# Kernel tuning notes

Measured on AMD Instinct MI355X. Metric: run time of the kernel, lower is better.

## Reference

```python
import jax, jax.numpy as jnp
import numpy as np

S, N_SUB, E_SUB = 64, 1024, 16384       # subgraphs, nodes/subgraph, edges/subgraph
N, E = 65536, 1048576                   # global nodes / edges
F_IN, NHID, NCLS, HEADS = 128, 128, 64, 2
RATIO = 0.5
K = int(np.ceil(RATIO * N_SUB))         # SAGPooling keeps K=512 nodes


def setup_inputs() -> dict:
    key = jax.random.key(0)
    ks = jax.random.split(key, 12)
    def lin(k, i, o):
        return jax.random.normal(k, (i, o), jnp.float32) / np.sqrt(i).astype(np.float32)
    return {
        'sub_x': jax.random.normal(ks[0], (S, N_SUB, F_IN), jnp.float32),
        'sub_edge_index': jax.random.randint(ks[1], (S, 2, E_SUB), 0, N_SUB, jnp.int32),
        'sub_orig_idx': jax.random.randint(ks[2], (S, N_SUB), 0, N, jnp.int32),
        'edge_index': jax.random.randint(ks[3], (2, E), 0, N, jnp.int32),
        'W1': lin(ks[4], F_IN, NHID), 'b1': jnp.zeros((NHID,), jnp.float32),
        'W2': lin(ks[5], NHID, NHID), 'b2': jnp.zeros((NHID,), jnp.float32),
        'Wp': lin(ks[6], NHID, 1), 'bp': jnp.zeros((1,), jnp.float32),
        'Wsc': lin(ks[7], NHID, NHID), 'bsc': jnp.zeros((NHID,), jnp.float32),
        'Wqkv': lin(ks[8], 2 * NHID, 6 * NHID), 'bqkv': jnp.zeros((6 * NHID,), jnp.float32),
        'Wo': lin(ks[9], 2 * NHID, 2 * NHID), 'bo': jnp.zeros((2 * NHID,), jnp.float32),
        'Wf': lin(ks[10], 3 * NHID, NCLS), 'bf': jnp.zeros((NCLS,), jnp.float32),
    }


def gcn(x, src, dst, ew, W, b, n):
    """PyG GCNConv: sym-normalized aggregation with self-loops; ew masks invalid edges."""
    h = x @ W
    deg = jax.ops.segment_sum(ew, dst, num_segments=n) + 1.0  # +1 self-loop
    dinv = jax.lax.rsqrt(deg)
    coef = dinv[src] * dinv[dst] * ew
    agg = jax.ops.segment_sum(h[src] * coef[:, None], dst, num_segments=n)
    return agg + h * (dinv * dinv)[:, None] + b


def _forward(sub_x, W1, b1, W2, b2, Wp, bp, Wsc, bsc, Wqkv, bqkv, Wo, bo, Wf, bf,
             sub_edge_index, sub_orig_idx, edge_index):
    dt = sub_x.dtype

    def cacos(x, ei):  # one subgraph: [N_SUB,F], [2,E_SUB]
        src, dst = ei[0], ei[1]
        ew1 = jnp.ones((E_SUB,), dt)
        x1 = jax.nn.relu(gcn(x, src, dst, ew1, W1, b1, N_SUB))
        x2 = jax.nn.relu(gcn(x1, src, dst, ew1, W2, b2, N_SUB))
        # SAGPooling on x1: GCN scorer -> top-k -> tanh gate
        score = gcn(x1, src, dst, ew1, Wp, bp, N_SUB)[:, 0]
        top_s, perm = jax.lax.top_k(score, K)
        x_pool = x1[perm] * jnp.tanh(top_s)[:, None]
        # remap edges to pooled indexing; invalid edges get weight 0
        pos = jnp.full((N_SUB,), -1, jnp.int32).at[perm].set(jnp.arange(K, dtype=jnp.int32))
        valid = (pos[src] >= 0) & (pos[dst] >= 0)
        psrc = jnp.where(valid, pos[src], 0)
        pdst = jnp.where(valid, pos[dst], 0)
        ew2 = valid.astype(dt)
        emb1 = jnp.concatenate([x_pool.max(0), x_pool.mean(0)])  # [2*NHID]
        x_sub = jax.nn.relu(gcn(x_pool, psrc, pdst, ew2, Wsc, bsc, K))
        emb2 = jnp.concatenate([x_sub.max(0), x_sub.mean(0)])
        return x2, emb1 + emb2

    node_embs, sub_embs = jax.vmap(cacos)(sub_x, sub_edge_index)  # [S,N_SUB,NHID], [S,2*NHID]

    # multi-head self-attention over subgraph embeddings (seq_len = 1 per the torch reshape)
    HD = (2 * NHID) // HEADS
    qkv = (sub_embs @ Wqkv + bqkv).reshape(S, 1, 3, HEADS, HD).transpose(2, 0, 3, 1, 4)
    q, k, v = qkv[0], qkv[1], qkv[2]                      # [S,H,1,HD]
    attn = jax.nn.softmax(jnp.einsum('shqd,shkd->shqk', q, k) / np.sqrt(HD).astype(np.float32), axis=-1)
    o = jnp.einsum('shqk,shkd->shqd', attn, v).transpose(0, 2, 1, 3).reshape(S, 1, 2 * NHID)
    att = (o @ Wo + bo)[:, 0]                             # [S, 2*NHID]

    # scatter-add per-node embeddings + broadcast subgraph embedding into global buffer
    combined = jnp.concatenate(
        [node_embs, jnp.broadcast_to(att[:, None, :], (S, N_SUB, 2 * NHID))], axis=-1)
    global_emb = jnp.zeros((N, 3 * NHID), dt).at[sub_orig_idx.reshape(-1)].add(
        combined.reshape(-1, 3 * NHID))

    logits = gcn(global_emb, edge_index[0], edge_index[1], jnp.ones((E,), dt), Wf, bf, N)
    return jax.nn.log_softmax(logits, axis=-1), global_emb


def reference(sub_x, sub_edge_index, sub_orig_idx, edge_index, W1, b1, W2, b2, Wp, bp,
              Wsc, bsc, Wqkv, bqkv, Wo, bo, Wf, bf):
    return _forward(sub_x, W1, b1, W2, b2, Wp, bp, Wsc, bsc, Wqkv, bqkv, Wo, bo, Wf, bf,
                    sub_edge_index, sub_orig_idx, edge_index)
```

## Files before the change

### kernel.cpp

```cpp
#include <hip/hip_runtime.h>
#include <math.h>

#define S     64
#define NSUB  1024
#define ESUB  16384
#define NG    65536
#define EG    1048576
#define NH    128
#define KSEL  512
#define BCAP  20480

__device__ __forceinline__ void mm1024_tile(const float* __restrict__ X,
        const float* __restrict__ W, float* __restrict__ Y, int row0, int t,
        float (*As)[136], float (*Bs)[136]) {
    int tr = t >> 5, tc = t & 31;
    float acc[4][4] = {};
    for (int k0 = 0; k0 < 128; k0 += 16) {
        if (t < 512) {
            int r = t >> 2, kq = t & 3;
            float4 v = *(const float4*)&X[(size_t)(row0 + r) * 128 + k0 + kq * 4];
            As[kq * 4 + 0][r] = v.x; As[kq * 4 + 1][r] = v.y;
            As[kq * 4 + 2][r] = v.z; As[kq * 4 + 3][r] = v.w;
        } else {
            int u = t - 512;
            int k = u >> 5, c = (u & 31) * 4;
            *(float4*)&Bs[k][c] = *(const float4*)&W[(size_t)(k0 + k) * 128 + c];
        }
        __syncthreads();
        #pragma unroll
        for (int k = 0; k < 16; k++) {
            float a0 = As[k][tr * 4 + 0], a1 = As[k][tr * 4 + 1];
            float a2 = As[k][tr * 4 + 2], a3 = As[k][tr * 4 + 3];
            float b0 = Bs[k][tc * 4 + 0], b1 = Bs[k][tc * 4 + 1];
            float b2 = Bs[k][tc * 4 + 2], b3 = Bs[k][tc * 4 + 3];
            acc[0][0] += a0 * b0; acc[0][1] += a0 * b1; acc[0][2] += a0 * b2; acc[0][3] += a0 * b3;
            acc[1][0] += a1 * b0; acc[1][1] += a1 * b1; acc[1][2] += a1 * b2; acc[1][3] += a1 * b3;
            acc[2][0] += a2 * b0; acc[2][1] += a2 * b1; acc[2][2] += a2 * b2; acc[2][3] += a2 * b3;
            acc[3][0] += a3 * b0; acc[3][1] += a3 * b1; acc[3][2] += a3 * b2; acc[3][3] += a3 * b3;
        }
        __syncthreads();
    }
    #pragma unroll
    for (int i = 0; i < 4; i++) {
        float4 v = { acc[i][0], acc[i][1], acc[i][2], acc[i][3] };
        *(float4*)&Y[(size_t)(row0 + tr * 4 + i) * 128 + tc * 4] = v;
    }
}

__global__ __launch_bounds__(1024) void k_csr_mm1(const int* __restrict__ sei,
        const int* __restrict__ sorig, int* __restrict__ rowptr, int* __restrict__ col,
        float* __restrict__ dinv, int* __restrict__ cntR,
        const float* __restrict__ X, const float* __restrict__ W, float* __restrict__ Y) {
    __shared__ float As[16][136];
    __shared__ float Bs[16][136];
    __shared__ int sh[1024];
    __shared__ int curL[1024];
    int b = blockIdx.x, t = threadIdx.x;
    if (b >= 128) {
        mm1024_tile(X, W, Y, (b - 128) * 128, t, As, Bs);
        return;
    }
    if (b >= 64) {
        int r = (b - 64) * 1024 + t;
        atomicAdd(&cntR[sorig[r]], 1);
        return;
    }
    int s = b;
    curL[t] = 0;
    __syncthreads();
    const int* dstp = sei + s * 2 * ESUB + ESUB;
    #pragma unroll
    for (int k = 0; k < 16; k++) atomicAdd(&curL[dstp[k * 1024 + t]], 1);
    __syncthreads();
    int v = curL[t];
    sh[t] = v;
    __syncthreads();
    for (int off = 1; off < 1024; off <<= 1) {
        int add = (t >= off) ? sh[t - off] : 0;
        __syncthreads();
        sh[t] += add;
        __syncthreads();
    }
    int incl = sh[t];
    int excl = incl - v;
    rowptr[s * (NSUB + 1) + t] = excl;
    dinv[s * NSUB + t] = rsqrtf((float)(v + 1));
    if (t == 1023) rowptr[s * (NSUB + 1) + NSUB] = incl;
    curL[t] = s * ESUB + excl;
    __syncthreads();
    const int* srcp = sei + s * 2 * ESUB;
    #pragma unroll
    for (int k = 0; k < 16; k++) {
        int e = k * 1024 + t;
        int src = srcp[e];
        int dst = dstp[e];
        int p = atomicAdd(&curL[dst], 1);
        col[p] = src;
    }
}

__global__ __launch_bounds__(1024) void k_scan_mm1(const int* __restrict__ cnt,
        int* __restrict__ rowptr, int* __restrict__ cur,
        const float* __restrict__ X, const float* __restrict__ W, float* __restrict__ Y) {
    __shared__ float As[16][136];
    __shared__ float Bs[16][136];
    __shared__ int sh[1024];
    __shared__ int wsum[16];
    __shared__ int sboff;
    int b = blockIdx.x, t = threadIdx.x;
    if (b >= 64) {
        mm1024_tile(X, W, Y, (b - 64 + 256) * 128, t, As, Bs);
        return;
    }
    int pre = 0;
    for (int i = t; i < b * 1024; i += 1024) pre += cnt[i];
    #pragma unroll
    for (int o = 32; o > 0; o >>= 1) pre += __shfl_xor(pre, o, 64);
    if ((t & 63) == 0) wsum[t >> 6] = pre;
    __syncthreads();
    if (t == 0) {
        int r = 0;
        #pragma unroll
        for (int i = 0; i < 16; i++) r += wsum[i];
        sboff = r;
    }
    int v = cnt[b * 1024 + t];
    sh[t] = v;
    __syncthreads();
    for (int off = 1; off < 1024; off <<= 1) {
        int add = (t >= off) ? sh[t - off] : 0;
        __syncthreads();
        sh[t] += add;
        __syncthreads();
    }
    int base = sboff;
    int r = base + sh[t] - v;
    int idx = b * 1024 + t;
    rowptr[idx] = r;
    cur[idx] = r;
    if (b == 63 && t == 1023) rowptr[NG] = base + sh[t];
}

__device__ __forceinline__ float4 agg_edges8(const float4* __restrict__ h, size_t hb,
        const int* __restrict__ cl, const float* __restrict__ dv,
        int st, int en, int f4) {
    float4 acc = {0.f, 0.f, 0.f, 0.f};
    int p = st;
    for (; p + 8 <= en; p += 8) {
        int s0 = cl[p + 0], s1 = cl[p + 1], s2 = cl[p + 2], s3 = cl[p + 3];
        int s4 = cl[p + 4], s5 = cl[p + 5], s6 = cl[p + 6], s7 = cl[p + 7];
        float d0 = dv[s0], d1 = dv[s1], d2 = dv[s2], d3 = dv[s3];
        float d4 = dv[s4], d5 = dv[s5], d6 = dv[s6], d7 = dv[s7];
        float4 h0 = h[(hb + s0) * 32 + f4];
        float4 h1 = h[(hb + s1) * 32 + f4];
        float4 h2 = h[(hb + s2) * 32 + f4];
        float4 h3 = h[(hb + s3) * 32 + f4];
        float4 h4 = h[(hb + s4) * 32 + f4];
        float4 h5 = h[(hb + s5) * 32 + f4];
        float4 h6 = h[(hb + s6) * 32 + f4];
        float4 h7 = h[(hb + s7) * 32 + f4];
        acc.x += h0.x * d0; acc.y += h0.y * d0; acc.z += h0.z * d0; acc.w += h0.w * d0;
        acc.x += h1.x * d1; acc.y += h1.y * d1; acc.z += h1.z * d1; acc.w += h1.w * d1;
        acc.x += h2.x * d2; acc.y += h2.y * d2; acc.z += h2.z * d2; acc.w += h2.w * d2;
        acc.x += h3.x * d3; acc.y += h3.y * d3; acc.z += h3.z * d3; acc.w += h3.w * d3;
        acc.x += h4.x * d4; acc.y += h4.y * d4; acc.z += h4.z * d4; acc.w += h4.w * d4;
        acc.x += h5.x * d5; acc.y += h5.y * d5; acc.z += h5.z * d5; acc.w += h5.w * d5;
        acc.x += h6.x * d6; acc.y += h6.y * d6; acc.z += h6.z * d6; acc.w += h6.w * d6;
        acc.x += h7.x * d7; acc.y += h7.y * d7; acc.z += h7.z * d7; acc.w += h7.w * d7;
    }
    for (; p + 4 <= en; p += 4) {
        int s0 = cl[p + 0], s1 = cl[p + 1], s2 = cl[p + 2], s3 = cl[p + 3];
        float d0 = dv[s0], d1 = dv[s1], d2 = dv[s2], d3 = dv[s3];
        float4 h0 = h[(hb + s0) * 32 + f4];
        float4 h1 = h[(hb + s1) * 32 + f4];
        float4 h2 = h[(hb + s2) * 32 + f4];
        float4 h3 = h[(hb + s3) * 32 + f4];
        acc.x += h0.x * d0; acc.y += h0.y * d0; acc.z += h0.z * d0; acc.w += h0.w * d0;
        acc.x += h1.x * d1; acc.y += h1.y * d1; acc.z += h1.z * d1; acc.w += h1.w * d1;
        acc.x += h2.x * d2; acc.y += h2.y * d2; acc.z += h2.z * d2; acc.w += h2.w * d2;
        acc.x += h3.x * d3; acc.y += h3.y * d3; acc.z += h3.z * d3; acc.w += h3.w * d3;
    }
    for (; p < en; p++) {
        int src = cl[p];
        float d = dv[src];
        float4 hv = h[(hb + src) * 32 + f4];
        acc.x += hv.x * d; acc.y += hv.y * d; acc.z += hv.z * d; acc.w += hv.w * d;
    }
    return acc;
}

__global__ __launch_bounds__(256) void k_mm2s(const float* __restrict__ X,
        const float* __restrict__ W, float* __restrict__ Y,
        const float* __restrict__ sh, const float* __restrict__ dinv,
        const int* __restrict__ rowptr, const int* __restrict__ col,
        const float* __restrict__ bp, float* __restrict__ score) {
    int t = threadIdx.x;
    if (blockIdx.x < 256) {
        int n = blockIdx.x * 256 + t;
        int s = n >> 10, nl = n & (NSUB - 1);
        const int* rp = rowptr + s * (NSUB + 1);
        const int* cl = col + s * ESUB;
        const float* dv = dinv + s * NSUB;
        const float* shs = sh + s * NSUB;
        int st = rp[nl], en = rp[nl + 1];
        float acc = 0.f;
        int p = st;
        for (; p + 8 <= en; p += 8) {
            int s0 = cl[p + 0], s1 = cl[p + 1], s2 = cl[p + 2], s3 = cl[p + 3];
            int s4 = cl[p + 4], s5 = cl[p + 5], s6 = cl[p + 6], s7 = cl[p + 7];
            float v0 = shs[s0] * dv[s0];
            float v1 = shs[s1] * dv[s1];
            float v2 = shs[s2] * dv[s2];
            float v3 = shs[s3] * dv[s3];
            float v4 = shs[s4] * dv[s4];
            float v5 = shs[s5] * dv[s5];
            float v6 = shs[s6] * dv[s6];
            float v7 = shs[s7] * dv[s7];
            acc += v0; acc += v1; acc += v2; acc += v3;
            acc += v4; acc += v5; acc += v6; acc += v7;
        }
        for (; p + 4 <= en; p += 4) {
            int s0 = cl[p + 0], s1 = cl[p + 1], s2 = cl[p + 2], s3 = cl[p + 3];
            float v0 = shs[s0] * dv[s0];
            float v1 = shs[s1] * dv[s1];
            float v2 = shs[s2] * dv[s2];
            float v3 = shs[s3] * dv[s3];
            acc += v0; acc += v1; acc += v2; acc += v3;
        }
        for (; p < en; p++) {
            int src = cl[p];
            acc += shs[src] * dv[src];
        }
        float dn = dv[nl];
        score[n] = acc * dn + sh[n] * dn * dn + bp[0];
        return;
    }
    __shared__ float As[16][72];
    __shared__ float Bs[16][72];
    int bb = blockIdx.x - 256;
    int row0 = (bb & 1023) * 64;
    int col0 = (bb >> 10) * 64;
    int tr = t >> 4, tc = t & 15;
    float acc[4][4] = {};
    for (int k0 = 0; k0 < 128; k0 += 16) {
        {   int r = t >> 2, kq = t & 3;
            float4 v = *(const float4*)&X[(size_t)(row0 + r) * 128 + k0 + kq * 4];
            As[kq * 4 + 0][r] = v.x; As[kq * 4 + 1][r] = v.y;
            As[kq * 4 + 2][r] = v.z; As[kq * 4 + 3][r] = v.w;
        }
        {   int k = t >> 4, cq = t & 15;
            float4 v = *(const float4*)&W[(size_t)(k0 + k) * 128 + col0 + cq * 4];
            *(float4*)&Bs[k][cq * 4] = v;
        }
        __syncthreads();
        #pragma unroll
        for (int k = 0; k < 16; k++) {
            float a0 = As[k][tr * 4 + 0], a1 = As[k][tr * 4 + 1];
            float a2 = As[k][tr * 4 + 2], a3 = As[k][tr * 4 + 3];
            float b0 = Bs[k][tc * 4 + 0], b1 = Bs[k][tc * 4 + 1];
            float b2 = Bs[k][tc * 4 + 2], b3 = Bs[k][tc * 4 + 3];
            acc[0][0] += a0 * b0; acc[0][1] += a0 * b1; acc[0][2] += a0 * b2; acc[0][3] += a0 * b3;
            acc[1][0] += a1 * b0; acc[1][1] += a1 * b1; acc[1][2] += a1 * b2; acc[1][3] += a1 * b3;
            acc[2][0] += a2 * b0; acc[2][1] += a2 * b1; acc[2][2] += a2 * b2; acc[2][3] += a2 * b3;
            acc[3][0] += a3 * b0; acc[3][1] += a3 * b1; acc[3][2] += a3 * b2; acc[3][3] += a3 * b3;
        }
        __syncthreads();
    }
    #pragma unroll
    for (int i = 0; i < 4; i++) {
        float4 v = { acc[i][0], acc[i][1], acc[i][2], acc[i][3] };
        *(float4*)&Y[(size_t)(row0 + tr * 4 + i) * 128 + col0 + tc * 4] = v;
    }
}

__global__ __launch_bounds__(256) void k_fillr_agg1(const int* __restrict__ orig,
        int* __restrict__ cur, int* __restrict__ rowlist, int* __restrict__ posR,
        const float4* __restrict__ h, const float* __restrict__ dinv,
        const int* __restrict__ rowptr, const int* __restrict__ col,
        const float* __restrict__ bias, const float* __restrict__ Wp,
        float4* __restrict__ out, float* __restrict__ scoreh) {
    int t = threadIdx.x;
    if (blockIdx.x < 256) {
        int r = blockIdx.x * 256 + t;
        int p = atomicAdd(&cur[orig[r]], 1);
        rowlist[p] = r;
        posR[r] = p;
        return;
    }
    int b = blockIdx.x - 256;
    int s = b & 63;
    int chunk = b >> 6;
    int nl = chunk * 8 + (t >> 5);
    int f4 = t & 31;
    const int* rp = rowptr + s * (NSUB + 1);
    int st = rp[nl], en = rp[nl + 1];
    float4 acc = agg_edges8(h, (size_t)s * NSUB, col + s * ESUB, dinv + s * NSUB, st, en, f4);
    size_t node = (size_t)s * NSUB + nl;
    const float* dv = dinv + s * NSUB;
    float dn = dv[nl];
    float dn2 = dn * dn;
    float4 hs = h[node * 32 + f4];
    float4 bb = ((const float4*)bias)[f4];
    float4 r;
    r.x = fmaxf(acc.x * dn + hs.x * dn2 + bb.x, 0.f);
    r.y = fmaxf(acc.y * dn + hs.y * dn2 + bb.y, 0.f);
    r.z = fmaxf(acc.z * dn + hs.z * dn2 + bb.z, 0.f);
    r.w = fmaxf(acc.w * dn + hs.w * dn2 + bb.w, 0.f);
    out[node * 32 + f4] = r;
    float4 wp = ((const float4*)Wp)[f4];
    float p = r.x * wp.x + r.y * wp.y + r.z * wp.z + r.w * wp.w;
    #pragma unroll
    for (int o = 16; o > 0; o >>= 1) p += __shfl_xor(p, o, 32);
    if (f4 == 0) scoreh[node] = p;
}

__global__ __launch_bounds__(512) void k_topk_agg2(const float4* __restrict__ h,
        const float* __restrict__ dinv, const int* __restrict__ rowptr,
        const int* __restrict__ col, const float* __restrict__ bias,
        const int* __restrict__ posR, float4* __restrict__ out,
        const float* __restrict__ score, int* __restrict__ perm,
        float* __restrict__ gate, int* __restrict__ posmap) {
    int t = threadIdx.x;
    if (blockIdx.x < 64) {
        __shared__ float sv[1024];
        __shared__ int   si[1024];
        int s = blockIdx.x;
        for (int i = t; i < 1024; i += 512) {
            sv[i] = score[s * NSUB + i];
            si[i] = i;
            posmap[s * NSUB + i] = -1;
        }
        __syncthreads();
        for (int k = 2; k <= 1024; k <<= 1) {
            for (int j = k >> 1; j > 0; j >>= 1) {
                for (int b = t; b < 1024; b += 512) {
                    int ixj = b ^ j;
                    if (ixj > b) {
                        bool desc = ((b & k) == 0);
                        bool sw = desc ? (sv[b] < sv[ixj]) : (sv[b] > sv[ixj]);
                        if (sw) {
                            float tv = sv[b]; sv[b] = sv[ixj]; sv[ixj] = tv;
                            int ti = si[b]; si[b] = si[ixj]; si[ixj] = ti;
                        }
                    }
                }
                __syncthreads();
            }
        }
        if (t < KSEL) {
            perm[s * KSEL + t] = si[t];
            gate[s * KSEL + t] = tanhf(sv[t]);
            posmap[s * NSUB + si[t]] = t;
        }
        return;
    }
    int b = blockIdx.x - 64;
    int s = b & 63;
    int chunk = b >> 6;
    int nl = chunk * 16 + (t >> 5);
    int f4 = t & 31;
    const int* rp = rowptr + s * (NSUB + 1);
    int st = rp[nl], en = rp[nl + 1];
    float4 acc = agg_edges8(h, (size_t)s * NSUB, col + s * ESUB, dinv + s * NSUB, st, en, f4);
    size_t node = (size_t)s * NSUB + nl;
    const float* dv = dinv + s * NSUB;
    float dn = dv[nl];
    float dn2 = dn * dn;
    float4 hs = h[node * 32 + f4];
    float4 bb = ((const float4*)bias)[f4];
    float4 r;
    r.x = fmaxf(acc.x * dn + hs.x * dn2 + bb.x, 0.f);
    r.y = fmaxf(acc.y * dn + hs.y * dn2 + bb.y, 0.f);
    r.z = fmaxf(acc.z * dn + hs.z * dn2 + bb.z, 0.f);
    r.w = fmaxf(acc.w * dn + hs.w * dn2 + bb.w, 0.f);
    out[(size_t)posR[node] * 32 + f4] = r;
}

__global__ __launch_bounds__(256) void k_pool(const float4* __restrict__ x1,
        const int* __restrict__ perm, const float* __restrict__ gate,
        const int* __restrict__ posmap, const int* __restrict__ rowptr,
        const int* __restrict__ col, float* __restrict__ dinv2,
        float4* __restrict__ xpool) {
    int t = threadIdx.x;
    int i = blockIdx.x * 8 + (t >> 5);
    int lane = t & 31;
    int s = i >> 9;
    int n = perm[i];
    const int* rp = rowptr + s * (NSUB + 1);
    const int* cl = col + s * ESUB;
    int st = rp[n], en = rp[n + 1];
    int c = 0;
    for (int p = st + lane; p < en; p += 32) c += (posmap[s * NSUB + cl[p]] >= 0) ? 1 : 0;
    #pragma unroll
    for (int o = 16; o > 0; o >>= 1) c += __shfl_xor(c, o, 32);
    if (lane == 0) dinv2[i] = rsqrtf((float)(c + 1));
    float g = gate[i];
    float4 v = x1[((size_t)(s * NSUB + n)) * 32 + lane];
    v.x *= g; v.y *= g; v.z *= g; v.w *= g;
    xpool[(size_t)i * 32 + lane] = v;
}

__global__ __launch_bounds__(1024) void k_emb_mmP(const float* __restrict__ X,
        float* __restrict__ out, const float* __restrict__ W, float* __restrict__ Y) {
    __shared__ float As[16][136];
    __shared__ float Bs[16][136];
    __shared__ float red[4][256];
    int b = blockIdx.x, t = threadIdx.x;
    if (b >= 64) {
        mm1024_tile(X, W, Y, (b - 64) * 128, t, As, Bs);
        return;
    }
    int s = b;
    int sl = t >> 8, f = t & 255;
    const float* base = X + (size_t)s * KSEL * NH;
    float r;
    if (f < NH) {
        r = -INFINITY;
        for (int i = sl * 128; i < sl * 128 + 128; i++) r = fmaxf(r, base[i * NH + f]);
    } else {
        r = 0.f;
        for (int i = sl * 128; i < sl * 128 + 128; i++) r += base[i * NH + (f - NH)];
    }
    red[sl][f] = r;
    __syncthreads();
    if (sl == 0) {
        float a = red[0][f], bb = red[1][f], c = red[2][f], d = red[3][f];
        float v = (f < NH) ? fmaxf(fmaxf(a, bb), fmaxf(c, d)) : (a + bb + c + d) * (1.f / KSEL);
        out[s * 256 + f] = v;
    }
}

__global__ __launch_bounds__(256) void k_aggp_bin(const float4* __restrict__ hp,
        const float* __restrict__ dinv2, const int* __restrict__ perm,
        const int* __restrict__ posmap, const int* __restrict__ rowptr,
        const int* __restrict__ col, const float* __restrict__ bsc,
        float4* __restrict__ xsub,
        const int* __restrict__ gei, int* __restrict__ bcur, int* __restrict__ ebin) {
    int t = threadIdx.x;
    if (blockIdx.x < 128) {
        __shared__ int lh[64];
        __shared__ int lbase[64];
        if (t < 64) lh[t] = 0;
        __syncthreads();
        int e0 = blockIdx.x * 8192;
        #pragma unroll 8
        for (int k = 0; k < 32; k++) {
            int d = gei[EG + e0 + k * 256 + t];
            atomicAdd(&lh[d >> 10], 1);
        }
        __syncthreads();
        if (t < 64) {
            lbase[t] = t * BCAP + atomicAdd(&bcur[t], lh[t]);
            lh[t] = 0;
        }
        __syncthreads();
        #pragma unroll 4
        for (int k = 0; k < 32; k++) {
            int idx = e0 + k * 256 + t;
            int d = gei[EG + idx];
            int src = gei[idx];
            int bb = d >> 10;
            int pos = lbase[bb] + atomicAdd(&lh[bb], 1);
            ebin[pos] = src | ((d & 1023) << 16);
        }
        return;
    }
    int b = blockIdx.x - 128;
    int s = b & 63;
    int chunk = b >> 6;
    int il = chunk * 8 + (t >> 5);
    int f4 = t & 31;
    int i = s * KSEL + il;
    int n = perm[i];
    const int* rp = rowptr + s * (NSUB + 1);
    const int* cl = col + s * ESUB;
    const int* pm = posmap + s * NSUB;
    const float* dv2 = dinv2 + s * KSEL;
    size_t hb = (size_t)s * KSEL;
    int st = rp[n], en = rp[n + 1];
    float4 acc = {0.f, 0.f, 0.f, 0.f};
    int p = st;
    for (; p + 8 <= en; p += 8) {
        int j0 = pm[cl[p + 0]], j1 = pm[cl[p + 1]], j2 = pm[cl[p + 2]], j3 = pm[cl[p + 3]];
        int j4 = pm[cl[p + 4]], j5 = pm[cl[p + 5]], j6 = pm[cl[p + 6]], j7 = pm[cl[p + 7]];
        int i0 = j0 >= 0 ? j0 : 0, i1 = j1 >= 0 ? j1 : 0;
        int i2 = j2 >= 0 ? j2 : 0, i3 = j3 >= 0 ? j3 : 0;
        int i4 = j4 >= 0 ? j4 : 0, i5 = j5 >= 0 ? j5 : 0;
        int i6 = j6 >= 0 ? j6 : 0, i7 = j7 >= 0 ? j7 : 0;
        float d0 = j0 >= 0 ? dv2[i0] : 0.f;
        float d1 = j1 >= 0 ? dv2[i1] : 0.f;
        float d2 = j2 >= 0 ? dv2[i2] : 0.f;
        float d3 = j3 >= 0 ? dv2[i3] : 0.f;
        float d4 = j4 >= 0 ? dv2[i4] : 0.f;
        float d5 = j5 >= 0 ? dv2[i5] : 0.f;
        float d6 = j6 >= 0 ? dv2[i6] : 0.f;
        float d7 = j7 >= 0 ? dv2[i7] : 0.f;
        float4 h0 = hp[(hb + i0) * 32 + f4];
        float4 h1 = hp[(hb + i1) * 32 + f4];
        float4 h2 = hp[(hb + i2) * 32 + f4];
        float4 h3 = hp[(hb + i3) * 32 + f4];
        float4 h4 = hp[(hb + i4) * 32 + f4];
        float4 h5 = hp[(hb + i5) * 32 + f4];
        float4 h6 = hp[(hb + i6) * 32 + f4];
        float4 h7 = hp[(hb + i7) * 32 + f4];
        acc.x += h0.x * d0; acc.y += h0.y * d0; acc.z += h0.z * d0; acc.w += h0.w * d0;
        acc.x += h1.x * d1; acc.y += h1.y * d1; acc.z += h1.z * d1; acc.w += h1.w * d1;
        acc.x += h2.x * d2; acc.y += h2.y * d2; acc.z += h2.z * d2; acc.w += h2.w * d2;
        acc.x += h3.x * d3; acc.y += h3.y * d3; acc.z += h3.z * d3; acc.w += h3.w * d3;
        acc.x += h4.x * d4; acc.y += h4.y * d4; acc.z += h4.z * d4; acc.w += h4.w * d4;
        acc.x += h5.x * d5; acc.y += h5.y * d5; acc.z += h5.z * d5; acc.w += h5.w * d5;
        acc.x += h6.x * d6; acc.y += h6.y * d6; acc.z += h6.z * d6; acc.w += h6.w * d6;
        acc.x += h7.x * d7; acc.y += h7.y * d7; acc.z += h7.z * d7; acc.w += h7.w * d7;
    }
    for (; p + 4 <= en; p += 4) {
        int j0 = pm[cl[p + 0]], j1 = pm[cl[p + 1]], j2 = pm[cl[p + 2]], j3 = pm[cl[p + 3]];
        int i0 = j0 >= 0 ? j0 : 0, i1 = j1 >= 0 ? j1 : 0;
        int i2 = j2 >= 0 ? j2 : 0, i3 = j3 >= 0 ? j3 : 0;
        float d0 = j0 >= 0 ? dv2[i0] : 0.f;
        float d1 = j1 >= 0 ? dv2[i1] : 0.f;
        float d2 = j2 >= 0 ? dv2[i2] : 0.f;
        float d3 = j3 >= 0 ? dv2[i3] : 0.f;
        float4 h0 = hp[(hb + i0) * 32 + f4];
        float4 h1 = hp[(hb + i1) * 32 + f4];
        float4 h2 = hp[(hb + i2) * 32 + f4];
        float4 h3 = hp[(hb + i3) * 32 + f4];
        acc.x += h0.x * d0; acc.y += h0.y * d0; acc.z += h0.z * d0; acc.w += h0.w * d0;
        acc.x += h1.x * d1; acc.y += h1.y * d1; acc.z += h1.z * d1; acc.w += h1.w * d1;
        acc.x += h2.x * d2; acc.y += h2.y * d2; acc.z += h2.z * d2; acc.w += h2.w * d2;
        acc.x += h3.x * d3; acc.y += h3.y * d3; acc.z += h3.z * d3; acc.w += h3.w * d3;
    }
    for (; p < en; p++) {
        int j = pm[cl[p]];
        if (j >= 0) {
            float d = dv2[j];
            float4 hv = hp[(hb + j) * 32 + f4];
            acc.x += hv.x * d; acc.y += hv.y * d; acc.z += hv.z * d; acc.w += hv.w * d;
        }
    }
    float dn = dinv2[i];
    float dn2 = dn * dn;
    float4 hs = hp[(size_t)i * 32 + f4];
    float4 bb = ((const float4*)bsc)[f4];
    float4 r;
    r.x = fmaxf(acc.x * dn + hs.x * dn2 + bb.x, 0.f);
    r.y = fmaxf(acc.y * dn + hs.y * dn2 + bb.y, 0.f);
    r.z = fmaxf(acc.z * dn + hs.z * dn2 + bb.z, 0.f);
    r.w = fmaxf(acc.w * dn + hs.w * dn2 + bb.w, 0.f);
    xsub[(size_t)i * 32 + f4] = r;
}

__global__ __launch_bounds__(1024) void k_ea_fb(const float* __restrict__ X,
        const float* __restrict__ subemb, const float* __restrict__ Wqkv,
        const float* __restrict__ bqkv, const float* __restrict__ Wo,
        const float* __restrict__ bo, const float* __restrict__ Wf,
        float* __restrict__ att, float* __restrict__ AW,
        const int* __restrict__ ebin, const int* __restrict__ bcur,
        int* __restrict__ rowptrN, float* __restrict__ dinvN, int* __restrict__ colN) {
    int t = threadIdx.x;
    if (blockIdx.x >= 64) {
        __shared__ int sh2[1024];
        __shared__ int curL[1024];
        __shared__ int sbase;
        int b = blockIdx.x - 64;
        if (t == 0) {
            int run = 0;
            for (int i = 0; i < b; i++) run += bcur[i];
            sbase = run;
        }
        curL[t] = 0;
        __syncthreads();
        int st = b * BCAP, en = st + bcur[b];
        for (int i = st + t; i < en; i += 1024) atomicAdd(&curL[ebin[i] >> 16], 1);
        __syncthreads();
        int v = curL[t];
        sh2[t] = v;
        __syncthreads();
        for (int off = 1; off < 1024; off <<= 1) {
            int add = (t >= off) ? sh2[t - off] : 0;
            __syncthreads();
            sh2[t] += add;
            __syncthreads();
        }
        int incl = sh2[t];
        int excl = incl - v;
        int base = sbase;
        rowptrN[(b << 10) + t] = base + excl;
        dinvN[(b << 10) + t] = rsqrtf((float)(v + 1));
        if (b == 63 && t == 1023) rowptrN[NG] = base + incl;
        curL[t] = base + excl;
        __syncthreads();
        for (int i = st + t; i < en; i += 1024) {
            int packed = ebin[i];
            int p = atomicAdd(&curL[packed >> 16], 1);
            colN[p] = packed & 0xFFFF;
        }
        return;
    }
    __shared__ float red[4][256];
    __shared__ float se[256], t1[256], av[256];
    int s = blockIdx.x;
    int sl = t >> 8, f = t & 255;
    const float* base = X + (size_t)s * KSEL * NH;
    float r;
    if (f < NH) {
        r = -INFINITY;
        for (int i = sl * 128; i < sl * 128 + 128; i++) r = fmaxf(r, base[i * NH + f]);
    } else {
        r = 0.f;
        for (int i = sl * 128; i < sl * 128 + 128; i++) r += base[i * NH + (f - NH)];
    }
    red[sl][f] = r;
    __syncthreads();
    if (sl == 0) {
        float a = red[0][f], b = red[1][f], c = red[2][f], d = red[3][f];
        float v = (f < NH) ? fmaxf(fmaxf(a, b), fmaxf(c, d)) : (a + b + c + d) * (1.f / KSEL);
        se[f] = subemb[s * 256 + f] + v;
    }
    __syncthreads();
    if (sl == 0) {
        float acc = bqkv[512 + f];
        for (int k = 0; k < 256; k++) acc += se[k] * Wqkv[(size_t)k * 768 + 512 + f];
        t1[f] = acc;
    }
    __syncthreads();
    if (sl == 0) {
        float a2 = bo[f];
        for (int k = 0; k < 256; k++) a2 += t1[k] * Wo[(size_t)k * 256 + f];
        att[s * 256 + f] = a2;
        av[f] = a2;
    }
    __syncthreads();
    if (sl == 0 && f < 64) {
        float acc = 0.f;
        for (int k = 0; k < 256; k++) acc += av[k] * Wf[(size_t)(NH + k) * 64 + f];
        AW[s * 64 + f] = acc;
    }
}

__global__ __launch_bounds__(256) void k_gx(const float4* __restrict__ x2s,
        const float4* __restrict__ att, const int* __restrict__ rowptrR,
        const int* __restrict__ rowlist, float4* __restrict__ gemb,
        const float* __restrict__ X, const float* __restrict__ W,
        const float* __restrict__ AW, float* __restrict__ Y) {
    int t = threadIdx.x;
    if (blockIdx.x >= NG / 64) {
        int g = (blockIdx.x - NG / 64) * 8 + (t >> 5);
        int lane = t & 31;
        int st = rowptrR[g], en = rowptrR[g + 1];
        float4 a0 = {0.f,0.f,0.f,0.f}, a1 = {0.f,0.f,0.f,0.f}, a2 = {0.f,0.f,0.f,0.f};
        for (int p = st; p < en; p++) {
            float4 v = x2s[(size_t)p * 32 + lane];
            a0.x += v.x; a0.y += v.y; a0.z += v.z; a0.w += v.w;
            int sub = rowlist[p] >> 10;
            float4 w1 = att[(size_t)sub * 64 + lane];
            float4 w2 = att[(size_t)sub * 64 + 32 + lane];
            a1.x += w1.x; a1.y += w1.y; a1.z += w1.z; a1.w += w1.w;
            a2.x += w2.x; a2.y += w2.y; a2.z += w2.z; a2.w += w2.w;
        }
        gemb[(size_t)g * 96 + lane]      = a0;
        gemb[(size_t)g * 96 + 32 + lane] = a1;
        gemb[(size_t)g * 96 + 64 + lane] = a2;
        return;
    }
    __shared__ float As[16][72];
    __shared__ float Bs[16][72];
    int row0 = blockIdx.x * 64;
    int tr = t >> 4, tc = t & 15;
    float acc[4][4] = {};
    for (int k0 = 0; k0 < 128; k0 += 16) {
        {   int r = t >> 2, kq = t & 3;
            float4 v = *(const float4*)&X[(size_t)(row0 + r) * 128 + k0 + kq * 4];
            As[kq * 4 + 0][r] = v.x; As[kq * 4 + 1][r] = v.y;
            As[kq * 4 + 2][r] = v.z; As[kq * 4 + 3][r] = v.w;
        }
        {   int k = t >> 4, cq = t & 15;
            float4 v = *(const float4*)&W[(size_t)(k0 + k) * 64 + cq * 4];
            *(float4*)&Bs[k][cq * 4] = v;
        }
        __syncthreads();
        #pragma unroll
        for (int k = 0; k < 16; k++) {
            float a0 = As[k][tr * 4 + 0], a1 = As[k][tr * 4 + 1];
            float a2 = As[k][tr * 4 + 2], a3 = As[k][tr * 4 + 3];
            float b0 = Bs[k][tc * 4 + 0], b1 = Bs[k][tc * 4 + 1];
            float b2 = Bs[k][tc * 4 + 2], b3 = Bs[k][tc * 4 + 3];
            acc[0][0] += a0 * b0; acc[0][1] += a0 * b1; acc[0][2] += a0 * b2; acc[0][3] += a0 * b3;
            acc[1][0] += a1 * b0; acc[1][1] += a1 * b1; acc[1][2] += a1 * b2; acc[1][3] += a1 * b3;
            acc[2][0] += a2 * b0; acc[2][1] += a2 * b1; acc[2][2] += a2 * b2; acc[2][3] += a2 * b3;
            acc[3][0] += a3 * b0; acc[3][1] += a3 * b1; acc[3][2] += a3 * b2; acc[3][3] += a3 * b3;
        }
        __syncthreads();
    }
    #pragma unroll
    for (int i = 0; i < 4; i++) {
        int rr = row0 + tr * 4 + i;
        int sub = rowlist[rr] >> 10;
        const float4 aw = *(const float4*)&AW[(size_t)sub * 64 + tc * 4];
        float4 v = { acc[i][0] + aw.x, acc[i][1] + aw.y, acc[i][2] + aw.z, acc[i][3] + aw.w };
        *(float4*)&Y[(size_t)rr * 64 + tc * 4] = v;
    }
}

__global__ __launch_bounds__(256) void k_gatherH(const float4* __restrict__ X2Ws,
        const int* __restrict__ rowptrR, float4* __restrict__ hf) {
    int t = threadIdx.x;
    int g = blockIdx.x * 16 + (t >> 4);
    int f4 = t & 15;
    int st = rowptrR[g], en = rowptrR[g + 1];
    float4 acc = {0.f, 0.f, 0.f, 0.f};
    for (int p = st; p < en; p++) {
        float4 a = X2Ws[(size_t)p * 16 + f4];
        acc.x += a.x; acc.y += a.y; acc.z += a.z; acc.w += a.w;
    }
    hf[(size_t)g * 16 + f4] = acc;
}

__global__ __launch_bounds__(256) void k_final(const float4* __restrict__ hf,
        const float* __restrict__ dinvN, const int* __restrict__ rowptr,
        const int* __restrict__ col, const float* __restrict__ bfb,
        float4* __restrict__ out) {
    int t = threadIdx.x;
    int n = blockIdx.x * 16 + (t >> 4);
    int f4 = t & 15;
    int st = rowptr[n], en = rowptr[n + 1];
    float4 acc = {0.f, 0.f, 0.f, 0.f};
    int p = st;
    for (; p + 8 <= en; p += 8) {
        int s0 = col[p + 0], s1 = col[p + 1], s2 = col[p + 2], s3 = col[p + 3];
        int s4 = col[p + 4], s5 = col[p + 5], s6 = col[p + 6], s7 = col[p + 7];
        float d0 = dinvN[s0], d1 = dinvN[s1], d2 = dinvN[s2], d3 = dinvN[s3];
        float d4 = dinvN[s4], d5 = dinvN[s5], d6 = dinvN[s6], d7 = dinvN[s7];
        float4 h0 = hf[(size_t)s0 * 16 + f4];
        float4 h1 = hf[(size_t)s1 * 16 + f4];
        float4 h2 = hf[(size_t)s2 * 16 + f4];
        float4 h3 = hf[(size_t)s3 * 16 + f4];
        float4 h4 = hf[(size_t)s4 * 16 + f4];
        float4 h5 = hf[(size_t)s5 * 16 + f4];
        float4 h6 = hf[(size_t)s6 * 16 + f4];
        float4 h7 = hf[(size_t)s7 * 16 + f4];
        acc.x += h0.x * d0; acc.y += h0.y * d0; acc.z += h0.z * d0; acc.w += h0.w * d0;
        acc.x += h1.x * d1; acc.y += h1.y * d1; acc.z += h1.z * d1; acc.w += h1.w * d1;
        acc.x += h2.x * d2; acc.y += h2.y * d2; acc.z += h2.z * d2; acc.w += h2.w * d2;
        acc.x += h3.x * d3; acc.y += h3.y * d3; acc.z += h3.z * d3; acc.w += h3.w * d3;
        acc.x += h4.x * d4; acc.y += h4.y * d4; acc.z += h4.z * d4; acc.w += h4.w * d4;
        acc.x += h5.x * d5; acc.y += h5.y * d5; acc.z += h5.z * d5; acc.w += h5.w * d5;
        acc.x += h6.x * d6; acc.y += h6.y * d6; acc.z += h6.z * d6; acc.w += h6.w * d6;
        acc.x += h7.x * d7; acc.y += h7.y * d7; acc.z += h7.z * d7; acc.w += h7.w * d7;
    }
    for (; p + 4 <= en; p += 4) {
        int s0 = col[p + 0], s1 = col[p + 1], s2 = col[p + 2], s3 = col[p + 3];
        float d0 = dinvN[s0], d1 = dinvN[s1], d2 = dinvN[s2], d3 = dinvN[s3];
        float4 h0 = hf[(size_t)s0 * 16 + f4];
        float4 h1 = hf[(size_t)s1 * 16 + f4];
        float4 h2 = hf[(size_t)s2 * 16 + f4];
        float4 h3 = hf[(size_t)s3 * 16 + f4];
        acc.x += h0.x * d0; acc.y += h0.y * d0; acc.z += h0.z * d0; acc.w += h0.w * d0;
        acc.x += h1.x * d1; acc.y += h1.y * d1; acc.z += h1.z * d1; acc.w += h1.w * d1;
        acc.x += h2.x * d2; acc.y += h2.y * d2; acc.z += h2.z * d2; acc.w += h2.w * d2;
        acc.x += h3.x * d3; acc.y += h3.y * d3; acc.z += h3.z * d3; acc.w += h3.w * d3;
    }
    for (; p < en; p++) {
        int src = col[p];
        float d = dinvN[src];
        float4 hv = hf[(size_t)src * 16 + f4];
        acc.x += hv.x * d; acc.y += hv.y * d; acc.z += hv.z * d; acc.w += hv.w * d;
    }
    float dn = dinvN[n];
    float dn2 = dn * dn;
    float4 hs = hf[(size_t)n * 16 + f4];
    float4 bb = ((const float4*)bfb)[f4];
    float4 x;
    x.x = acc.x * dn + hs.x * dn2 + bb.x;
    x.y = acc.y * dn + hs.y * dn2 + bb.y;
    x.z = acc.z * dn + hs.z * dn2 + bb.z;
    x.w = acc.w * dn + hs.w * dn2 + bb.w;
    float m = fmaxf(fmaxf(x.x, x.y), fmaxf(x.z, x.w));
    for (int o = 1; o < 16; o <<= 1) m = fmaxf(m, __shfl_xor(m, o, 64));
    float ssum = expf(x.x - m) + expf(x.y - m) + expf(x.z - m) + expf(x.w - m);
    for (int o = 1; o < 16; o <<= 1) ssum += __shfl_xor(ssum, o, 64);
    float lz = m + logf(ssum);
    float4 r = { x.x - lz, x.y - lz, x.z - lz, x.w - lz };
    out[(size_t)n * 16 + f4] = r;
}

extern "C" void kernel_launch(void* const* d_in, const int* in_sizes, int n_in,
                              void* d_out, int out_size, void* d_ws, size_t ws_size,
                              hipStream_t stream) {
    const float* sub_x = (const float*)d_in[0];
    const int*   sei   = (const int*)d_in[1];
    const int*   sorig = (const int*)d_in[2];
    const int*   gei   = (const int*)d_in[3];
    const float *W1 = (const float*)d_in[4],  *b1  = (const float*)d_in[5];
    const float *W2 = (const float*)d_in[6],  *b2  = (const float*)d_in[7];
    const float *Wp = (const float*)d_in[8],  *bp  = (const float*)d_in[9];
    const float *Wsc = (const float*)d_in[10], *bsc = (const float*)d_in[11];
    const float *Wqkv = (const float*)d_in[12], *bqkv = (const float*)d_in[13];
    const float *Wo = (const float*)d_in[14], *bo  = (const float*)d_in[15];
    const float *Wf = (const float*)d_in[16], *bfb = (const float*)d_in[17];

    float* out0 = (float*)d_out;
    float* gemb = (float*)d_out + (size_t)NG * 64;

    char* w = (char*)d_ws;
    size_t off = 0;
    auto alloc = [&](size_t nbytes) -> void* {
        off = (off + 255) & ~(size_t)255;
        void* p = w + off;
        off += nbytes;
        return p;
    };
    int*   bcur    = (int*)alloc(64 * 4);
    int*   cntR    = (int*)alloc((size_t)NG * 4);
    float* AW      = (float*)alloc((size_t)S * 64 * 4);
    float* dinv    = (float*)alloc((size_t)NG * 4);
    float* scoreh  = (float*)alloc((size_t)NG * 4);
    float* score   = (float*)alloc((size_t)NG * 4);
    float* gate    = (float*)alloc((size_t)S * KSEL * 4);
    float* dinv2   = (float*)alloc((size_t)S * KSEL * 4);
    float* subemb  = (float*)alloc((size_t)S * 256 * 4);
    float* att     = (float*)alloc((size_t)S * 256 * 4);
    int*   perm    = (int*)alloc((size_t)S * KSEL * 4);
    int*   posmap  = (int*)alloc((size_t)NG * 4);
    int*   cur_sub = (int*)alloc((size_t)NG * 4);
    int*   rowptr_s= (int*)alloc((size_t)(NG + 64) * 4);
    int*   col_sub = (int*)alloc((size_t)EG * 4);
    int*   rowptrR = (int*)alloc((size_t)(NG + 64) * 4);
    int*   rowlist = (int*)alloc((size_t)NG * 4);
    int*   posR    = (int*)alloc((size_t)NG * 4);
    float* x1      = (float*)alloc((size_t)NG * NH * 4);
    float* x2s     = (float*)alloc((size_t)NG * NH * 4);
    float* hbuf    = (float*)alloc((size_t)NG * NH * 4);
    float* xpool   = (float*)alloc((size_t)S * KSEL * NH * 4);
    float* xsub    = x1;
    float* hf      = hbuf;
    float* dinvN   = dinv;
    float* X2Ws    = x1;
    int*   curR    = cur_sub;
    int*   rowptrN = rowptr_s;
    int*   colN    = col_sub;
    int*   ebin    = (int*)xpool;

    hipMemsetAsync(bcur, 0, 256 + (size_t)NG * 4, stream);

    k_csr_mm1<<<384, 1024, 0, stream>>>(sei, sorig, rowptr_s, col_sub, dinv, cntR,
                                        sub_x, W1, hbuf);
    k_scan_mm1<<<320, 1024, 0, stream>>>(cntR, rowptrR, curR, sub_x, W1, hbuf);

    k_fillr_agg1<<<256 + 8192, 256, 0, stream>>>(sorig, curR, rowlist, posR,
                                                 (const float4*)hbuf, dinv, rowptr_s, col_sub,
                                                 b1, Wp, (float4*)x1, scoreh);
    k_mm2s<<<256 + 2048, 256, 0, stream>>>(x1, W2, hbuf,
                                           scoreh, dinv, rowptr_s, col_sub, bp, score);
    k_topk_agg2<<<64 + 4096, 512, 0, stream>>>((const float4*)hbuf, dinv, rowptr_s, col_sub,
                                               b2, posR, (float4*)x2s,
                                               score, perm, gate, posmap);
    k_pool<<<(S * KSEL) / 8, 256, 0, stream>>>((const float4*)x1, perm, gate, posmap,
                                               rowptr_s, col_sub, dinv2, (float4*)xpool);
    k_emb_mmP<<<64 + (S * KSEL) / 128, 1024, 0, stream>>>(xpool, subemb, Wsc, hbuf);
    k_aggp_bin<<<128 + 4096, 256, 0, stream>>>((const float4*)hbuf, dinv2, perm, posmap,
                                               rowptr_s, col_sub, bsc, (float4*)xsub,
                                               gei, bcur, ebin);
    k_ea_fb<<<128, 1024, 0, stream>>>(xsub, subemb, Wqkv, bqkv, Wo, bo, Wf, att, AW,
                                      ebin, bcur, rowptrN, dinvN, colN);
    k_gx<<<NG / 64 + NG / 8, 256, 0, stream>>>((const float4*)x2s, (const float4*)att,
                                               rowptrR, rowlist, (float4*)gemb,
                                               x2s, Wf, AW, X2Ws);
    k_gatherH<<<NG / 16, 256, 0, stream>>>((const float4*)X2Ws, rowptrR, (float4*)hf);

    k_final<<<NG / 16, 256, 0, stream>>>((const float4*)hf, dinvN, rowptrN, colN, bfb, (float4*)out0);

    (void)in_sizes; (void)n_in; (void)out_size; (void)ws_size;
}
```

Before: 586.2 us.

## Enlarge mm2 tiles to 128x128 and stage subgraph features in LDS for agg2

The second GEMM in k_mm2s now uses 128-row by full-width tiles with an 8x8 register micro-tile per thread, where it used 64x64 tiles with 4x4. This cuts the block count and the repeated loads of X and W. The second GCN aggregation in k_topk_agg2 now loads one subgraph's 16-feature slice into shared memory. Each thread then aggregates whole nodes from LDS instead of gathering from global memory per edge. The cost is fewer blocks (512), serial per-thread edge loops with load imbalance, 64 KB of LDS per block which limits occupancy, and more register pressure in the GEMM.

```diff
diff --git a/kernel.cpp b/kernel.cpp
--- a/kernel.cpp
+++ b/kernel.cpp
@@ -235,41 +235,49 @@
         score[n] = acc * dn + sh[n] * dn * dn + bp[0];
         return;
     }
-    __shared__ float As[16][72];
-    __shared__ float Bs[16][72];
-    int bb = blockIdx.x - 256;
-    int row0 = (bb & 1023) * 64;
-    int col0 = (bb >> 10) * 64;
+    __shared__ float As[16][136];
+    __shared__ float Bs[16][136];
+    int row0 = (blockIdx.x - 256) * 128;
     int tr = t >> 4, tc = t & 15;
-    float acc[4][4] = {};
+    float acc[8][8] = {};
     for (int k0 = 0; k0 < 128; k0 += 16) {
-        {   int r = t >> 2, kq = t & 3;
-            float4 v = *(const float4*)&X[(size_t)(row0 + r) * 128 + k0 + kq * 4];
-            As[kq * 4 + 0][r] = v.x; As[kq * 4 + 1][r] = v.y;
-            As[kq * 4 + 2][r] = v.z; As[kq * 4 + 3][r] = v.w;
-        }
-        {   int k = t >> 4, cq = t & 15;
-            float4 v = *(const float4*)&W[(size_t)(k0 + k) * 128 + col0 + cq * 4];
-            *(float4*)&Bs[k][cq * 4] = v;
+        {
+            int r = t >> 1, half = t & 1;
+            const float* xp = &X[(size_t)(row0 + r) * 128 + k0 + half * 8];
+            float4 v0 = *(const float4*)xp;
+            float4 v1 = *(const float4*)(xp + 4);
+            int kb = half * 8;
+            As[kb + 0][r] = v0.x; As[kb + 1][r] = v0.y; As[kb + 2][r] = v0.z; As[kb + 3][r] = v0.w;
+            As[kb + 4][r] = v1.x; As[kb + 5][r] = v1.y; As[kb + 6][r] = v1.z; As[kb + 7][r] = v1.w;
+        }
+        {
+            int k = t >> 4, c = (t & 15) * 4;
+            *(float4*)&Bs[k][c]      = *(const float4*)&W[(size_t)(k0 + k) * 128 + c];
+            *(float4*)&Bs[k][c + 64] = *(const float4*)&W[(size_t)(k0 + k) * 128 + c + 64];
         }
         __syncthreads();
         #pragma unroll
         for (int k = 0; k < 16; k++) {
-            float a0 = As[k][tr * 4 + 0], a1 = As[k][tr * 4 + 1];
-            float a2 = As[k][tr * 4 + 2], a3 = As[k][tr * 4 + 3];
-            float b0 = Bs[k][tc * 4 + 0], b1 = Bs[k][tc * 4 + 1];
-            float b2 = Bs[k][tc * 4 + 2], b3 = Bs[k][tc * 4 + 3];
-            acc[0][0] += a0 * b0; acc[0][1] += a0 * b1; acc[0][2] += a0 * b2; acc[0][3] += a0 * b3;
-            acc[1][0] += a1 * b0; acc[1][1] += a1 * b1; acc[1][2] += a1 * b2; acc[1][3] += a1 * b3;
-            acc[2][0] += a2 * b0; acc[2][1] += a2 * b1; acc[2][2] += a2 * b2; acc[2][3] += a2 * b3;
-            acc[3][0] += a3 * b0; acc[3][1] += a3 * b1; acc[3][2] += a3 * b2; acc[3][3] += a3 * b3;
+            float a[8], b[8];
+            *(float4*)&a[0] = *(const float4*)&As[k][tr * 8];
+            *(float4*)&a[4] = *(const float4*)&As[k][tr * 8 + 4];
+            *(float4*)&b[0] = *(const float4*)&Bs[k][tc * 8];
+            *(float4*)&b[4] = *(const float4*)&Bs[k][tc * 8 + 4];
+            #pragma unroll
+            for (int i = 0; i < 8; i++)
+                #pragma unroll
+                for (int j = 0; j < 8; j++)
+                    acc[i][j] += a[i] * b[j];
         }
         __syncthreads();
     }
     #pragma unroll
-    for (int i = 0; i < 4; i++) {
-        float4 v = { acc[i][0], acc[i][1], acc[i][2], acc[i][3] };
-        *(float4*)&Y[(size_t)(row0 + tr * 4 + i) * 128 + col0 + tc * 4] = v;
+    for (int i = 0; i < 8; i++) {
+        float4 v0 = { acc[i][0], acc[i][1], acc[i][2], acc[i][3] };
+        float4 v1 = { acc[i][4], acc[i][5], acc[i][6], acc[i][7] };
+        float* yp = &Y[(size_t)(row0 + tr * 8 + i) * 128 + tc * 8];
+        *(float4*)yp = v0;
+        *(float4*)(yp + 4) = v1;
     }
 }
 
@@ -320,10 +328,11 @@
         const int* __restrict__ posR, float4* __restrict__ out,
         const float* __restrict__ score, int* __restrict__ perm,
         float* __restrict__ gate, int* __restrict__ posmap) {
+    __shared__ float smem[16384];
     int t = threadIdx.x;
     if (blockIdx.x < 64) {
-        __shared__ float sv[1024];
-        __shared__ int   si[1024];
+        float* sv = smem;
+        int*   si = (int*)(smem + 1024);
         int s = blockIdx.x;
         for (int i = t; i < 1024; i += 512) {
             sv[i] = score[s * NSUB + i];
@@ -356,24 +365,60 @@
     }
     int b = blockIdx.x - 64;
     int s = b & 63;
-    int chunk = b >> 6;
-    int nl = chunk * 16 + (t >> 5);
-    int f4 = t & 31;
+    int q = b >> 6;
+    float4* lds4 = (float4*)smem;
+    const float4* hsub = h + (size_t)s * NSUB * 32;
+    for (int idx = t; idx < 4096; idx += 512) {
+        int row = idx >> 2, j = idx & 3;
+        lds4[j * 1024 + row] = hsub[(size_t)row * 32 + q * 4 + j];
+    }
+    __syncthreads();
     const int* rp = rowptr + s * (NSUB + 1);
-    int st = rp[nl], en = rp[nl + 1];
-    float4 acc = agg_edges8(h, (size_t)s * NSUB, col + s * ESUB, dinv + s * NSUB, st, en, f4);
-    size_t node = (size_t)s * NSUB + nl;
+    const int* cl = col + s * ESUB;
     const float* dv = dinv + s * NSUB;
-    float dn = dv[nl];
-    float dn2 = dn * dn;
-    float4 hs = h[node * 32 + f4];
-    float4 bb = ((const float4*)bias)[f4];
-    float4 r;
-    r.x = fmaxf(acc.x * dn + hs.x * dn2 + bb.x, 0.f);
-    r.y = fmaxf(acc.y * dn + hs.y * dn2 + bb.y, 0.f);
-    r.z = fmaxf(acc.z * dn + hs.z * dn2 + bb.z, 0.f);
-    r.w = fmaxf(acc.w * dn + hs.w * dn2 + bb.w, 0.f);
-    out[(size_t)posR[node] * 32 + f4] = r;
+    const float4* bb4 = (const float4*)bias + q * 4;
+    for (int nl = t; nl < NSUB; nl += 512) {
+        int st = rp[nl], en = rp[nl + 1];
+        float4 a0 = {0.f,0.f,0.f,0.f}, a1 = {0.f,0.f,0.f,0.f};
+        float4 a2 = {0.f,0.f,0.f,0.f}, a3 = {0.f,0.f,0.f,0.f};
+        for (int p = st; p < en; p++) {
+            int src = cl[p];
+            float d = dv[src];
+            float4 v0 = lds4[src];
+            float4 v1 = lds4[1024 + src];
+            float4 v2 = lds4[2048 + src];
+            float4 v3 = lds4[3072 + src];
+            a0.x += v0.x * d; a0.y += v0.y * d; a0.z += v0.z * d; a0.w += v0.w * d;
+            a1.x += v1.x * d; a1.y += v1.y * d; a1.z += v1.z * d; a1.w += v1.w * d;
+            a2.x += v2.x * d; a2.y += v2.y * d; a2.z += v2.z * d; a2.w += v2.w * d;
+            a3.x += v3.x * d; a3.y += v3.y * d; a3.z += v3.z * d; a3.w += v3.w * d;
+        }
+        float dn = dv[nl];
+        float dn2 = dn * dn;
+        float4 h0 = lds4[nl], h1 = lds4[1024 + nl], h2 = lds4[2048 + nl], h3 = lds4[3072 + nl];
+        size_t orow = (size_t)posR[s * NSUB + nl] * 32 + q * 4;
+        float4 r0, r1, r2, r3;
+        r0.x = fmaxf(a0.x * dn + h0.x * dn2 + bb4[0].x, 0.f);
+        r0.y = fmaxf(a0.y * dn + h0.y * dn2 + bb4[0].y, 0.f);
+        r0.z = fmaxf(a0.z * dn + h0.z * dn2 + bb4[0].z, 0.f);
+        r0.w = fmaxf(a0.w * dn + h0.w * dn2 + bb4[0].w, 0.f);
+        r1.x = fmaxf(a1.x * dn + h1.x * dn2 + bb4[1].x, 0.f);
+        r1.y = fmaxf(a1.y * dn + h1.y * dn2 + bb4[1].y, 0.f);
+        r1.z = fmaxf(a1.z * dn + h1.z * dn2 + bb4[1].z, 0.f);
+        r1.w = fmaxf(a1.w * dn + h1.w * dn2 + bb4[1].w, 0.f);
+        r2.x = fmaxf(a2.x * dn + h2.x * dn2 + bb4[2].x, 0.f);
+        r2.y = fmaxf(a2.y * dn + h2.y * dn2 + bb4[2].y, 0.f);
+        r2.z = fmaxf(a2.z * dn + h2.z * dn2 + bb4[2].z, 0.f);
+        r2.w = fmaxf(a2.w * dn + h2.w * dn2 + bb4[2].w, 0.f);
+        r3.x = fmaxf(a3.x * dn + h3.x * dn2 + bb4[3].x, 0.f);
+        r3.y = fmaxf(a3.y * dn + h3.y * dn2 + bb4[3].y, 0.f);
+        r3.z = fmaxf(a3.z * dn + h3.z * dn2 + bb4[3].z, 0.f);
+        r3.w = fmaxf(a3.w * dn + h3.w * dn2 + bb4[3].w, 0.f);
+        out[orow + 0] = r0;
+        out[orow + 1] = r1;
+        out[orow + 2] = r2;
+        out[orow + 3] = r3;
+    }
 }
 
 __global__ __launch_bounds__(256) void k_pool(const float4* __restrict__ x1,
@@ -849,11 +894,11 @@
     k_fillr_agg1<<<256 + 8192, 256, 0, stream>>>(sorig, curR, rowlist, posR,
                                                  (const float4*)hbuf, dinv, rowptr_s, col_sub,
                                                  b1, Wp, (float4*)x1, scoreh);
-    k_mm2s<<<256 + 2048, 256, 0, stream>>>(x1, W2, hbuf,
-                                           scoreh, dinv, rowptr_s, col_sub, bp, score);
-    k_topk_agg2<<<64 + 4096, 512, 0, stream>>>((const float4*)hbuf, dinv, rowptr_s, col_sub,
-                                               b2, posR, (float4*)x2s,
-                                               score, perm, gate, posmap);
+    k_mm2s<<<256 + 512, 256, 0, stream>>>(x1, W2, hbuf,
+                                          scoreh, dinv, rowptr_s, col_sub, bp, score);
+    k_topk_agg2<<<64 + 512, 512, 0, stream>>>((const float4*)hbuf, dinv, rowptr_s, col_sub,
+                                              b2, posR, (float4*)x2s,
+                                              score, perm, gate, posmap);
     k_pool<<<(S * KSEL) / 8, 256, 0, stream>>>((const float4*)x1, perm, gate, posmap,
                                                rowptr_s, col_sub, dinv2, (float4*)xpool);
     k_emb_mmP<<<64 + (S * KSEL) / 128, 1024, 0, stream>>>(xpool, subemb, Wsc, hbuf);
```

Result: no change. 588.9 us (+0.5%).
